# Performance work log

Hardware: AMD Instinct MI355X
Metric: run time of the kernel (lower is better)

## Reference

```python
import jax, jax.numpy as jnp
import numpy as np
import math

N_NEURONS = 2048
TAU_MEM = 10.0
TAU_SYN = 5.0
V_TH = 1.0
V_RESET = 0.0
ALPHA_MEM = math.exp(-1.0 / TAU_MEM)
ALPHA_SYN = math.exp(-1.0 / TAU_SYN)


def setup_inputs() -> dict:
    key = jax.random.key(0)
    B, T, N = 8, 1024, N_NEURONS
    x = jax.random.normal(key, (B, T, N), dtype=jnp.float32)
    membrane = jnp.zeros((B, N), dtype=jnp.float32)
    trace = jnp.zeros((B, N), dtype=jnp.float32)
    return {"x": x, "membrane": membrane, "trace": trace}


def reference(x, membrane, trace):
    """StatefulLIF.forward_sequence: LIF recurrence over T via lax.scan.

    x: [B, T, N]; membrane, trace: [B, N].
    Returns (spikes [B, T, N], final_membrane [B, N], final_trace [B, N]).
    """
    a_m = jnp.asarray(ALPHA_MEM, x.dtype)
    a_s = jnp.asarray(ALPHA_SYN, x.dtype)
    reset_amt = jnp.asarray(V_TH - V_RESET, x.dtype)

    def step(carry, x_t):
        m, tr = carry
        m = a_m * m + (1 - a_m) * x_t
        s = (m > V_TH).astype(x_t.dtype)  # Heaviside spike
        m = m - reset_amt * s
        tr = a_s * tr + s
        return (m, tr), s

    # scan over time: move T to leading axis
    (m_f, tr_f), spikes_t = jax.lax.scan(step, (membrane, trace), jnp.swapaxes(x, 0, 1))
    spikes = jnp.swapaxes(spikes_t, 0, 1)  # [B, T, N]
    return spikes, m_f, tr_f
```

## Files before the change

### kernel.cpp

```cpp
#include <hip/hip_runtime.h>


#define LIF_B 8
#define LIF_T 1024
#define LIF_N 2048

#define A_MEM 0.90483741803595952f
#define A_SYN 0.81873075307798185f

#define CHUNK 64
#define NCHUNK (LIF_T / CHUNK)

#define BARRIER()                                  \
  do {                                             \
    __asm__ __volatile__("" ::: "memory");         \
    __builtin_amdgcn_s_barrier();                  \
    __asm__ __volatile__("" ::: "memory");         \
  } while (0)

__global__ __launch_bounds__(128) void lif_pc_kernel(
    const float* __restrict__ x,
    const float* __restrict__ m0,
    const float* __restrict__ tr0,
    float* __restrict__ out) {
  __shared__ float xbuf[2][CHUNK][64];

  const int wid = threadIdx.x >> 6;
  const int l   = threadIdx.x & 63;
  const int chain = blockIdx.x * 64 + l;
  const int b = chain >> 11;
  const int n = chain & (LIF_N - 1);
  const size_t plane = (size_t)LIF_T * LIF_N;
  const float* __restrict__ xp = x + (size_t)b * plane + n;

  if (wid == 0) {
    #pragma unroll
    for (int j = 0; j < CHUNK; ++j) {
      __builtin_amdgcn_global_load_lds(
          (const __attribute__((address_space(1))) void*)(xp + (size_t)j * LIF_N),
          (__attribute__((address_space(3))) void*)(&xbuf[0][j][0]),
          4, 0, 0);
    }
    __asm__ __volatile__("s_waitcnt vmcnt(0)" ::: "memory");
  }

  float m = 0.f, tr = 0.f;
  float* sp = nullptr;
  if (wid == 1) {
    m  = m0[chain];
    tr = tr0[chain];
    sp = out + (size_t)b * plane + n;
  }

  BARRIER();

  constexpr float am   = A_MEM;
  constexpr float as   = A_SYN;
  constexpr float onem = 1.0f - A_MEM;

  #pragma unroll 1
  for (int c = 0; c < NCHUNK; ++c) {
    if (wid == 0) {
      if (c + 1 < NCHUNK) {
        const float* g = xp + (size_t)(c + 1) * CHUNK * LIF_N;
        #pragma unroll
        for (int j = 0; j < CHUNK; ++j) {
          __builtin_amdgcn_global_load_lds(
              (const __attribute__((address_space(1))) void*)(g + (size_t)j * LIF_N),
              (__attribute__((address_space(3))) void*)(&xbuf[(c + 1) & 1][j][0]),
              4, 0, 0);
        }
      }
      __asm__ __volatile__("s_waitcnt vmcnt(0)" ::: "memory");
    } else {
      float xr[CHUNK];
      #pragma unroll
      for (int j = 0; j < CHUNK; ++j) xr[j] = xbuf[c & 1][j][l];
      float* spc = sp + (size_t)c * CHUNK * LIF_N;
      #pragma unroll
      for (int j = 0; j < CHUNK; ++j) {
        m = fmaf(am, m, onem * xr[j]);
        float s_ = (m > 1.0f) ? 1.0f : 0.0f;
        m -= s_;
        tr = fmaf(as, tr, s_);
        __builtin_nontemporal_store(s_, spc + (size_t)j * LIF_N);
      }
    }
    BARRIER();
  }

  if (wid == 1) {
    float* mf  = out + (size_t)LIF_B * plane;
    float* trf = mf + (size_t)LIF_B * LIF_N;
    mf[chain]  = m;
    trf[chain] = tr;
  }
}

extern "C" void kernel_launch(void* const* d_in, const int* in_sizes, int n_in,
                              void* d_out, int out_size, void* d_ws, size_t ws_size,
                              hipStream_t stream) {
  const float* x   = (const float*)d_in[0];
  const float* m0  = (const float*)d_in[1];
  const float* tr0 = (const float*)d_in[2];
  float* out = (float*)d_out;

  const int grid = (LIF_B * LIF_N) / 64;
  lif_pc_kernel<<<grid, 128, 0, stream>>>(x, m0, tr0, out);
}
```

Baseline: 123.7 us.

## Deepen LDS prefetch to four buffers and use 16-byte global-to-LDS loads

The producer wave now keeps three chunks of input in flight using a four-deep LDS ring, with partial vmcnt waits instead of draining to zero every chunk. Each global_load_lds now moves 16 bytes per lane covering four timesteps per instruction, cutting load instruction count by four. This hides more memory latency at the cost of 64KB of LDS per block, which may lower occupancy. It also adds more complex wait-count bookkeeping.

```diff
diff --git a/kernel.cpp b/kernel.cpp
--- a/kernel.cpp
+++ b/kernel.cpp
@@ -10,6 +10,8 @@
 
 #define CHUNK 64
 #define NCHUNK (LIF_T / CHUNK)
+#define NBUF 4
+#define LPC 16
 
 #define BARRIER()                                  \
   do {                                             \
@@ -18,38 +20,50 @@
     __asm__ __volatile__("" ::: "memory");         \
   } while (0)
 
+#define WAITV(n) __asm__ __volatile__("s_waitcnt vmcnt(" #n ")" ::: "memory")
+
 __global__ __launch_bounds__(128) void lif_pc_kernel(
     const float* __restrict__ x,
     const float* __restrict__ m0,
     const float* __restrict__ tr0,
     float* __restrict__ out) {
-  __shared__ float xbuf[2][CHUNK][64];
+  __shared__ float xbuf[NBUF][CHUNK][64];
 
   const int wid = threadIdx.x >> 6;
   const int l   = threadIdx.x & 63;
-  const int chain = blockIdx.x * 64 + l;
-  const int b = chain >> 11;
-  const int n = chain & (LIF_N - 1);
+  const int b   = blockIdx.x >> 5;
+  const int n0  = (blockIdx.x * 64) & (LIF_N - 1);
   const size_t plane = (size_t)LIF_T * LIF_N;
-  const float* __restrict__ xp = x + (size_t)b * plane + n;
 
-  if (wid == 0) {
-    #pragma unroll
-    for (int j = 0; j < CHUNK; ++j) {
-      __builtin_amdgcn_global_load_lds(
-          (const __attribute__((address_space(1))) void*)(xp + (size_t)j * LIF_N),
-          (__attribute__((address_space(3))) void*)(&xbuf[0][j][0]),
-          4, 0, 0);
-    }
-    __asm__ __volatile__("s_waitcnt vmcnt(0)" ::: "memory");
-  }
+  const float* __restrict__ gl =
+      x + (size_t)b * plane + (size_t)(l >> 4) * LIF_N + n0 + 4 * (l & 15);
+
+  #define ISSUE_CHUNK(cc)                                                    \
+    do {                                                                     \
+      const float* g_ = gl + (size_t)(cc) * CHUNK * LIF_N;                   \
+      float(*lb_)[64] = xbuf[(cc) & (NBUF - 1)];                             \
+      _Pragma("unroll")                                                      \
+      for (int i_ = 0; i_ < LPC; ++i_) {                                     \
+        __builtin_amdgcn_global_load_lds(                                    \
+            (const __attribute__((address_space(1))) void*)(                 \
+                g_ + (size_t)(4 * i_) * LIF_N),                              \
+            (__attribute__((address_space(3))) void*)(&lb_[4 * i_][0]),      \
+            16, 0, 0);                                                       \
+      }                                                                      \
+    } while (0)
 
   float m = 0.f, tr = 0.f;
   float* sp = nullptr;
-  if (wid == 1) {
+  if (wid == 0) {
+    ISSUE_CHUNK(0);
+    ISSUE_CHUNK(1);
+    ISSUE_CHUNK(2);
+    WAITV(32);
+  } else {
+    const int chain = blockIdx.x * 64 + l;
     m  = m0[chain];
     tr = tr0[chain];
-    sp = out + (size_t)b * plane + n;
+    sp = out + (size_t)b * plane + n0 + l;
   }
 
   BARRIER();
@@ -61,21 +75,19 @@
   #pragma unroll 1
   for (int c = 0; c < NCHUNK; ++c) {
     if (wid == 0) {
-      if (c + 1 < NCHUNK) {
-        const float* g = xp + (size_t)(c + 1) * CHUNK * LIF_N;
-        #pragma unroll
-        for (int j = 0; j < CHUNK; ++j) {
-          __builtin_amdgcn_global_load_lds(
-              (const __attribute__((address_space(1))) void*)(g + (size_t)j * LIF_N),
-              (__attribute__((address_space(3))) void*)(&xbuf[(c + 1) & 1][j][0]),
-              4, 0, 0);
-        }
+      if (c + 3 < NCHUNK) {
+        ISSUE_CHUNK(c + 3);
+        WAITV(32);
+      } else if (c == NCHUNK - 3) {
+        WAITV(16);
+      } else if (c == NCHUNK - 2) {
+        WAITV(0);
       }
-      __asm__ __volatile__("s_waitcnt vmcnt(0)" ::: "memory");
     } else {
       float xr[CHUNK];
+      float(*lb)[64] = xbuf[c & (NBUF - 1)];
       #pragma unroll
-      for (int j = 0; j < CHUNK; ++j) xr[j] = xbuf[c & 1][j][l];
+      for (int j = 0; j < CHUNK; ++j) xr[j] = lb[j][l];
       float* spc = sp + (size_t)c * CHUNK * LIF_N;
       #pragma unroll
       for (int j = 0; j < CHUNK; ++j) {
@@ -88,8 +100,10 @@
     }
     BARRIER();
   }
+  #undef ISSUE_CHUNK
 
   if (wid == 1) {
+    const int chain = blockIdx.x * 64 + l;
     float* mf  = out + (size_t)LIF_B * plane;
     float* trf = mf + (size_t)LIF_B * LIF_N;
     mf[chain]  = m;
```

New measurement: 123.4 us. No clear change (-0.2%).
